# Performance work log

Measured on AMD Instinct MI355X. Metric: run time of the kernel, lower is better.

The kernel has to match this reference:

```python
import jax, jax.numpy as jnp
import numpy as np

NUM_HEADS = 8
NEG_SLOPE = 0.2


def setup_inputs() -> dict:
    key = jax.random.key(0)
    k1, k2, k3, k4 = jax.random.split(key, 4)
    B, N, D_IN, D_K, D_V = 4, 4096, 256, 256, 256
    x = jax.random.normal(k1, (B, N, D_IN), dtype=jnp.float32)
    Wq = jax.random.normal(k2, (D_IN, D_K), dtype=jnp.float32) * (1.0 / np.sqrt(D_IN))
    Wk = jax.random.normal(k3, (D_IN, D_K), dtype=jnp.float32) * (1.0 / np.sqrt(D_IN))
    Wv = jax.random.normal(k4, (D_IN, D_V), dtype=jnp.float32) * (1.0 / np.sqrt(D_IN))
    return {"x": x, "Wq": Wq, "Wk": Wk, "Wv": Wv}


def reference(x, Wq, Wk, Wv):
    B, N, _ = x.shape
    nh = NUM_HEADS
    dim_k = Wq.shape[1]
    dim_v = Wv.shape[1]
    dk, dv = dim_k // nh, dim_v // nh
    nor_fact = 1.0 / np.sqrt(dk)
    # project and split heads: [B, H, N, dk]
    q = (x @ Wq).reshape(B, N, nh, dk).transpose(0, 2, 1, 3)
    k = (x @ Wk).reshape(B, N, nh, dk).transpose(0, 2, 1, 3)
    v = (x @ Wv).reshape(B, N, nh, dv).transpose(0, 2, 1, 3)
    # all-pairs scores, scaled then LeakyReLU (no softmax)
    dist = jnp.einsum('bhnd,bhmd->bhnm', q, k) * nor_fact
    dist = jnp.where(dist >= 0, dist, NEG_SLOPE * dist)
    att = jnp.einsum('bhnm,bhmd->bhnd', dist, v)
    return att.transpose(0, 2, 1, 3).reshape(B, N, dim_v)
```

## Files before the change

### kernel.cpp

```cpp
#include <hip/hip_runtime.h>

typedef __attribute__((ext_vector_type(8))) short short8;
typedef __attribute__((ext_vector_type(4))) float f32x4;
typedef __attribute__((ext_vector_type(2))) unsigned int u32x2;
typedef __attribute__((ext_vector_type(4))) unsigned int u32x4;

#define MFMA16x32(A, B, C) \
  __builtin_amdgcn_mfma_f32_16x16x32_bf16((A), (B), (C), 0, 0, 0)

__device__ __forceinline__ void async_cp16(const unsigned short* g, void* l) {
  __builtin_amdgcn_global_load_lds(
      (const __attribute__((address_space(1))) unsigned int*)g,
      (__attribute__((address_space(3))) unsigned int*)l, 16, 0, 0);
}

__device__ __forceinline__ unsigned int fbits(float f) {
  return __builtin_bit_cast(unsigned int, f);
}
__device__ __forceinline__ unsigned int pack_bf16(float a, float b) {
  return __builtin_amdgcn_perm(fbits(b), fbits(a), 0x07060302u);
}
__device__ __forceinline__ unsigned short bf16_rne(float f) {
  unsigned int u = fbits(f);
  return (unsigned short)((u + 0x8000u) >> 16);
}

__global__ __launch_bounds__(256) void prep_kernel(
    const float* __restrict__ x, unsigned short* __restrict__ xb,
    const float* __restrict__ Wq, const float* __restrict__ Wk,
    const float* __restrict__ Wv, unsigned short* __restrict__ WT) {
  __shared__ float tile[32][33];
  if (blockIdx.x < 4096) {
    const size_t i = ((size_t)blockIdx.x * 256 + threadIdx.x) * 4;
    const float4 f = *(const float4*)(x + i);
    u32x2 u = {(unsigned int)bf16_rne(f.x) | ((unsigned int)bf16_rne(f.y) << 16),
               (unsigned int)bf16_rne(f.z) | ((unsigned int)bf16_rne(f.w) << 16)};
    *(u32x2*)(xb + i) = u;
    return;
  }
  const int bid = blockIdx.x - 4096;
  const int g = bid / 64, rem = bid % 64;
  const int k0 = (rem >> 3) * 32, n0 = (rem & 7) * 32;
  const float* W = (g == 0) ? Wq : (g == 1) ? Wk : Wv;
  const int t = threadIdx.x;
  {
    const int kr = t >> 3, nc = (t & 7) * 4;
    const float4 f = *(const float4*)(W + (size_t)(k0 + kr) * 256 + n0 + nc);
    tile[kr][nc + 0] = f.x; tile[kr][nc + 1] = f.y;
    tile[kr][nc + 2] = f.z; tile[kr][nc + 3] = f.w;
  }
  __syncthreads();
  {
    const int nr = t >> 3, kc = (t & 7) * 4;
    unsigned int u0 = (unsigned int)bf16_rne(tile[kc + 0][nr]) |
                      ((unsigned int)bf16_rne(tile[kc + 1][nr]) << 16);
    unsigned int u1 = (unsigned int)bf16_rne(tile[kc + 2][nr]) |
                      ((unsigned int)bf16_rne(tile[kc + 3][nr]) << 16);
    u32x2 u = {u0, u1};
    *(u32x2*)(WT + (size_t)g * 65536 + (size_t)(n0 + nr) * 256 + k0 + kc) = u;
  }
}

__global__ __launch_bounds__(256, 2) void proj_kernel(
    const unsigned short* __restrict__ xb, const unsigned short* __restrict__ WT,
    unsigned short* __restrict__ QH, unsigned short* __restrict__ KH,
    unsigned short* __restrict__ VT) {
  __shared__ __align__(16) char smem[65536];
  const int tid = threadIdx.x;
  const int w = tid >> 6, lane = tid & 63, l15 = lane & 15, quad = lane >> 4;
  const int bid = blockIdx.x;
  const int mtile = bid / 6, nt = bid % 6;
  const int g = nt >> 1, n0 = (nt & 1) * 128;
  const int m0 = mtile * 128;

  const int srow = lane >> 3, useg = lane & 7;
  const int swz = (useg ^ srow) * 8;
  const unsigned short* aS = xb + (size_t)(m0 + w * 32 + srow) * 256 + swz;
  const unsigned short* bS =
      WT + (size_t)g * 65536 + (size_t)(n0 + w * 32 + srow) * 256 + swz;

#pragma unroll
  for (int j = 0; j < 4; j++) {
    async_cp16(aS + j * 2048, smem + w * 4096 + j * 1024);
    async_cp16(bS + j * 2048, smem + 16384 + w * 4096 + j * 1024);
  }
  __syncthreads();

  const f32x4 zero = {0.f, 0.f, 0.f, 0.f};
  f32x4 acc[2][8];
#pragma unroll
  for (int s = 0; s < 2; s++)
#pragma unroll
    for (int c = 0; c < 8; c++) acc[s][c] = zero;

  const int sw = l15 & 7;
  for (int t = 0; t < 4; t++) {
    const int nb = t & 1;
    const int kn = ((t + 1) & 3) * 64;
#pragma unroll
    for (int j = 0; j < 4; j++) {
      async_cp16(aS + kn + j * 2048,
                 smem + (nb ^ 1) * 32768 + w * 4096 + j * 1024);
      async_cp16(bS + kn + j * 2048,
                 smem + (nb ^ 1) * 32768 + 16384 + w * 4096 + j * 1024);
    }
    const char* Ab = smem + nb * 32768;
    const char* Bb = Ab + 16384;
#pragma unroll
    for (int ks = 0; ks < 2; ks++) {
      const int seg = ((ks * 4 + quad) ^ sw) * 16;
      short8 af[2], bf[8];
#pragma unroll
      for (int s = 0; s < 2; s++)
        af[s] = *(const short8*)(Ab + (w * 32 + s * 16 + l15) * 128 + seg);
#pragma unroll
      for (int c = 0; c < 8; c++)
        bf[c] = *(const short8*)(Bb + (c * 16 + l15) * 128 + seg);
      if (g < 2) {
#pragma unroll
        for (int s = 0; s < 2; s++)
#pragma unroll
          for (int c = 0; c < 8; c++)
            acc[s][c] = MFMA16x32(bf[c], af[s], acc[s][c]);
      } else {
#pragma unroll
        for (int s = 0; s < 2; s++)
#pragma unroll
          for (int c = 0; c < 8; c++)
            acc[s][c] = MFMA16x32(af[s], bf[c], acc[s][c]);
      }
    }
    __syncthreads();
  }

  if (g < 2) {
    unsigned short* O = g ? KH : QH;
    const float sc = g ? 1.0f : 0.17677669529663688f;
#pragma unroll
    for (int s = 0; s < 2; s++)
#pragma unroll
      for (int c = 0; c < 8; c++) {
        const int row = m0 + w * 32 + s * 16 + l15;
        const int col = n0 + c * 16 + quad * 4;
        const int bb = row >> 12, nn = row & 4095;
        const int hh = col >> 5, dl = col & 31;
        u32x2 pk = {pack_bf16(acc[s][c][0] * sc, acc[s][c][1] * sc),
                    pack_bf16(acc[s][c][2] * sc, acc[s][c][3] * sc)};
        *(u32x2*)(O + ((size_t)(bb * 8 + hh) * 4096 + nn) * 32 + dl) = pk;
      }
  } else {
#pragma unroll
    for (int s = 0; s < 2; s++)
#pragma unroll
      for (int c = 0; c < 8; c++) {
        const int col = n0 + c * 16 + l15;
        const int hh = col >> 5, dl = col & 31;
        const int row = m0 + w * 32 + s * 16 + quad * 4;
        const int bb = row >> 12;
        const int nn = (row & 4064) | (quad << 3) | ((s & 1) << 2);
        u32x2 pk = {pack_bf16(acc[s][c][0], acc[s][c][1]),
                    pack_bf16(acc[s][c][2], acc[s][c][3])};
        *(u32x2*)(VT + (size_t)((bb * 8 + hh) * 32 + dl) * 4096 + nn) = pk;
      }
  }
}

__global__ __launch_bounds__(512, 4) void attn_kernel(
    const unsigned short* __restrict__ QH, const unsigned short* __restrict__ KH,
    const unsigned short* __restrict__ VT, float* __restrict__ out) {
  __shared__ __align__(16) char smem[16384];
  const int tid = threadIdx.x;
  const int w = tid >> 6, lane = tid & 63, l15 = lane & 15, quad = lane >> 4;
  const int bid = blockIdx.x;
  const int bh = bid & 31, qh = bid >> 5;
  const int b = bh >> 3, h = bh & 7;
  const int qbase = qh * 256 + w * 32;

  const unsigned short* Qp =
      QH + ((size_t)bh * 4096 + qbase + l15) * 32 + quad * 8;
  short8 qf[2];
#pragma unroll
  for (int s = 0; s < 2; s++) qf[s] = *(const short8*)(Qp + (size_t)s * 512);

  const bool isK = (w < 4);
  const unsigned short* src0;
  int kstr, wbOff;
  if (isK) {
    const int key = w * 16 + (lane >> 2);
    const int gseg = (lane & 3) ^ ((lane >> 3) & 3);
    src0 = KH + ((size_t)bh * 4096 + key) * 32 + gseg * 8;
    kstr = 32;
    wbOff = w * 1024;
  } else {
    const int r = (w - 4) * 8 + (lane >> 3), useg = lane & 7;
    src0 = VT + ((size_t)bh * 32 + r) * 4096 + ((useg ^ (r & 7)) * 8);
    kstr = 1;
    wbOff = 4096 + (w - 4) * 1024;
  }

  async_cp16(src0, smem + wbOff);
  __syncthreads();

  const f32x4 zero = {0.f, 0.f, 0.f, 0.f};
  f32x4 acc[2][2];
#pragma unroll
  for (int s = 0; s < 2; s++) {
    acc[s][0] = zero;
    acc[s][1] = zero;
  }

  const int rs = l15 & 7;
  const int kseg = (quad ^ ((l15 >> 1) & 3)) * 16;
  for (int i = 0; i < 64; i++) {
    const int nb = i & 1;
    const int kn = ((i + 1) & 63) * 64;
    async_cp16(src0 + (size_t)kn * kstr, smem + (nb ^ 1) * 8192 + wbOff);

    const char* Kb = smem + nb * 8192;
    const char* Vb = Kb + 4096;
    short8 kf[4];
#pragma unroll
    for (int c = 0; c < 4; c++)
      kf[c] = *(const short8*)(Kb + (c * 16 + l15) * 64 + kseg);
    short8 vf[2][2];
#pragma unroll
    for (int dt = 0; dt < 2; dt++) {
      const char* Vr = Vb + (dt * 16 + l15) * 128;
#pragma unroll
      for (int u = 0; u < 2; u++)
        vf[dt][u] = *(const short8*)(Vr + (((4 * u + quad) ^ rs) * 16));
    }

#pragma unroll
    for (int s = 0; s < 2; s++) {
      unsigned int pp[4][2];
#pragma unroll
      for (int c = 0; c < 4; c++) {
        f32x4 st = MFMA16x32(kf[c], qf[s], zero);
        float t0 = fmaxf(st[0], 0.2f * st[0]);
        float t1 = fmaxf(st[1], 0.2f * st[1]);
        float t2 = fmaxf(st[2], 0.2f * st[2]);
        float t3 = fmaxf(st[3], 0.2f * st[3]);
        pp[c][0] = pack_bf16(t0, t1);
        pp[c][1] = pack_bf16(t2, t3);
      }
#pragma unroll
      for (int u = 0; u < 2; u++) {
        u32x4 bw = {pp[2 * u][0], pp[2 * u][1],
                    pp[2 * u + 1][0], pp[2 * u + 1][1]};
        short8 pb = __builtin_bit_cast(short8, bw);
#pragma unroll
        for (int dt = 0; dt < 2; dt++)
          acc[s][dt] = MFMA16x32(vf[dt][u], pb, acc[s][dt]);
      }
    }
    __syncthreads();
  }

#pragma unroll
  for (int s = 0; s < 2; s++)
#pragma unroll
    for (int dt = 0; dt < 2; dt++)
      *(f32x4*)(out + ((size_t)b * 4096 + qbase + s * 16 + l15) * 256 + h * 32 +
                dt * 16 + quad * 4) = acc[s][dt];
}

extern "C" void kernel_launch(void* const* d_in, const int* in_sizes, int n_in,
                              void* d_out, int out_size, void* d_ws,
                              size_t ws_size, hipStream_t stream) {
  const float* x = (const float*)d_in[0];
  const float* Wq = (const float*)d_in[1];
  const float* Wk = (const float*)d_in[2];
  const float* Wv = (const float*)d_in[3];
  float* out = (float*)d_out;

  unsigned short* ws = (unsigned short*)d_ws;
  unsigned short* QHb = ws;
  unsigned short* KHb = ws + 4194304;
  unsigned short* VTb = ws + 2 * 4194304;
  unsigned short* xbb = ws + 3 * 4194304;
  unsigned short* WTb = ws + 4 * 4194304;

  prep_kernel<<<4288, 256, 0, stream>>>(x, xbb, Wq, Wk, Wv, WTb);
  proj_kernel<<<768, 256, 0, stream>>>(xbb, WTb, QHb, KHb, VTb);
  attn_kernel<<<512, 512, 0, stream>>>(QHb, KHb, VTb, out);
}
```

Before: 168.6 us.

## Halve per-wave query rows in attention, double grid, raise occupancy bound

Each wave of the attention kernel now covers 16 query rows instead of 32. The grid doubles to 1024 blocks and the launch bound targets 8 blocks per CU. LeakyReLU is also rewritten as a packed 2-wide multiply and max before the bf16 pack. The aim is more parallelism and better latency hiding, but every block now streams all K/V tiles for half as many queries. That doubles K/V global and LDS traffic per unit of work and halves MFMA reuse of each loaded K/V fragment.

```diff
diff --git a/kernel.cpp b/kernel.cpp
--- a/kernel.cpp
+++ b/kernel.cpp
@@ -2,6 +2,7 @@
 
 typedef __attribute__((ext_vector_type(8))) short short8;
 typedef __attribute__((ext_vector_type(4))) float f32x4;
+typedef __attribute__((ext_vector_type(2))) float f32x2;
 typedef __attribute__((ext_vector_type(2))) unsigned int u32x2;
 typedef __attribute__((ext_vector_type(4))) unsigned int u32x4;
 
@@ -23,6 +24,12 @@
 __device__ __forceinline__ unsigned short bf16_rne(float f) {
   unsigned int u = fbits(f);
   return (unsigned short)((u + 0x8000u) >> 16);
+}
+__device__ __forceinline__ unsigned int leaky_pack(float a, float b) {
+  f32x2 v = {a, b};
+  f32x2 m = v * 0.2f;
+  f32x2 r = __builtin_elementwise_max(v, m);
+  return pack_bf16(r[0], r[1]);
 }
 
 __global__ __launch_bounds__(256) void prep_kernel(
@@ -165,7 +172,7 @@
   }
 }
 
-__global__ __launch_bounds__(512, 4) void attn_kernel(
+__global__ __launch_bounds__(512, 8) void attn_kernel(
     const unsigned short* __restrict__ QH, const unsigned short* __restrict__ KH,
     const unsigned short* __restrict__ VT, float* __restrict__ out) {
   __shared__ __align__(16) char smem[16384];
@@ -174,13 +181,11 @@
   const int bid = blockIdx.x;
   const int bh = bid & 31, qh = bid >> 5;
   const int b = bh >> 3, h = bh & 7;
-  const int qbase = qh * 256 + w * 32;
+  const int qbase = qh * 128 + w * 16;
 
   const unsigned short* Qp =
       QH + ((size_t)bh * 4096 + qbase + l15) * 32 + quad * 8;
-  short8 qf[2];
-#pragma unroll
-  for (int s = 0; s < 2; s++) qf[s] = *(const short8*)(Qp + (size_t)s * 512);
+  const short8 qf = *(const short8*)Qp;
 
   const bool isK = (w < 4);
   const unsigned short* src0;
@@ -202,12 +207,9 @@
   __syncthreads();
 
   const f32x4 zero = {0.f, 0.f, 0.f, 0.f};
-  f32x4 acc[2][2];
-#pragma unroll
-  for (int s = 0; s < 2; s++) {
-    acc[s][0] = zero;
-    acc[s][1] = zero;
-  }
+  f32x4 acc[2];
+  acc[0] = zero;
+  acc[1] = zero;
 
   const int rs = l15 & 7;
   const int kseg = (quad ^ ((l15 >> 1) & 3)) * 16;
@@ -231,38 +233,29 @@
         vf[dt][u] = *(const short8*)(Vr + (((4 * u + quad) ^ rs) * 16));
     }
 
-#pragma unroll
-    for (int s = 0; s < 2; s++) {
-      unsigned int pp[4][2];
-#pragma unroll
-      for (int c = 0; c < 4; c++) {
-        f32x4 st = MFMA16x32(kf[c], qf[s], zero);
-        float t0 = fmaxf(st[0], 0.2f * st[0]);
-        float t1 = fmaxf(st[1], 0.2f * st[1]);
-        float t2 = fmaxf(st[2], 0.2f * st[2]);
-        float t3 = fmaxf(st[3], 0.2f * st[3]);
-        pp[c][0] = pack_bf16(t0, t1);
-        pp[c][1] = pack_bf16(t2, t3);
-      }
-#pragma unroll
-      for (int u = 0; u < 2; u++) {
-        u32x4 bw = {pp[2 * u][0], pp[2 * u][1],
-                    pp[2 * u + 1][0], pp[2 * u + 1][1]};
-        short8 pb = __builtin_bit_cast(short8, bw);
-#pragma unroll
-        for (int dt = 0; dt < 2; dt++)
-          acc[s][dt] = MFMA16x32(vf[dt][u], pb, acc[s][dt]);
-      }
+    unsigned int pp[4][2];
+#pragma unroll
+    for (int c = 0; c < 4; c++) {
+      f32x4 st = MFMA16x32(kf[c], qf, zero);
+      pp[c][0] = leaky_pack(st[0], st[1]);
+      pp[c][1] = leaky_pack(st[2], st[3]);
+    }
+#pragma unroll
+    for (int u = 0; u < 2; u++) {
+      u32x4 bw = {pp[2 * u][0], pp[2 * u][1],
+                  pp[2 * u + 1][0], pp[2 * u + 1][1]};
+      short8 pb = __builtin_bit_cast(short8, bw);
+#pragma unroll
+      for (int dt = 0; dt < 2; dt++)
+        acc[dt] = MFMA16x32(vf[dt][u], pb, acc[dt]);
     }
     __syncthreads();
   }
 
 #pragma unroll
-  for (int s = 0; s < 2; s++)
-#pragma unroll
-    for (int dt = 0; dt < 2; dt++)
-      *(f32x4*)(out + ((size_t)b * 4096 + qbase + s * 16 + l15) * 256 + h * 32 +
-                dt * 16 + quad * 4) = acc[s][dt];
+  for (int dt = 0; dt < 2; dt++)
+    *(f32x4*)(out + ((size_t)b * 4096 + qbase + l15) * 256 + h * 32 +
+              dt * 16 + quad * 4) = acc[dt];
 }
 
 extern "C" void kernel_launch(void* const* d_in, const int* in_sizes, int n_in,
@@ -283,5 +276,5 @@
 
   prep_kernel<<<4288, 256, 0, stream>>>(x, xbb, Wq, Wk, Wv, WTb);
   proj_kernel<<<768, 256, 0, stream>>>(xbb, WTb, QHb, KHb, VTb);
-  attn_kernel<<<512, 512, 0, stream>>>(QHb, KHb, VTb, out);
-}
+  attn_kernel<<<1024, 512, 0, stream>>>(QHb, KHb, VTb, out);
+}
```

Result: slower. 185.6 us (+10.1%).

## Decompose LeakyReLU into ReLU plus linear term via precomputed V^T K

Applied to the files above, without the earlier changes.

Rewrites LeakyReLU(s) as 0.8*ReLU(s) + 0.2*s. The linear part is computed once per block as q·(K^T V) from a 32x32 matrix M that every block builds from the full K and V, and the inner loop then needs only a packed-bf16 integer max against zero. This cuts the per-score VALU work (multiply, max, separate pack) down to pack plus one packed max. The cost is that each block re-reads all of K and V for its head to build M, using strided scalar K loads, a larger shared buffer, and extra syncs.

```diff
diff --git a/kernel.cpp b/kernel.cpp
--- a/kernel.cpp
+++ b/kernel.cpp
@@ -23,6 +23,11 @@
 __device__ __forceinline__ unsigned short bf16_rne(float f) {
   unsigned int u = fbits(f);
   return (unsigned short)((u + 0x8000u) >> 16);
+}
+__device__ __forceinline__ unsigned int relu_pk_bf16(unsigned int x) {
+  unsigned int r;
+  asm("v_pk_max_i16 %0, %1, 0" : "=v"(r) : "v"(x));
+  return r;
 }
 
 __global__ __launch_bounds__(256) void prep_kernel(
@@ -168,7 +173,7 @@
 __global__ __launch_bounds__(512, 4) void attn_kernel(
     const unsigned short* __restrict__ QH, const unsigned short* __restrict__ KH,
     const unsigned short* __restrict__ VT, float* __restrict__ out) {
-  __shared__ __align__(16) char smem[16384];
+  __shared__ __align__(16) char smem[32768];
   const int tid = threadIdx.x;
   const int w = tid >> 6, lane = tid & 63, l15 = lane & 15, quad = lane >> 4;
   const int bid = blockIdx.x;
@@ -181,6 +186,67 @@
   short8 qf[2];
 #pragma unroll
   for (int s = 0; s < 2; s++) qf[s] = *(const short8*)(Qp + (size_t)s * 512);
+
+  const f32x4 zero = {0.f, 0.f, 0.f, 0.f};
+
+  float* Mred = (float*)smem;
+  {
+    f32x4 mm[2][2];
+#pragma unroll
+    for (int dt = 0; dt < 2; dt++)
+#pragma unroll
+      for (int it = 0; it < 2; it++) mm[dt][it] = zero;
+    const unsigned short* Vg = VT + ((size_t)bh * 32 + l15) * 4096 + quad * 8;
+    const unsigned short* Kg = KH + ((size_t)bh * 4096) * 32 + l15;
+    for (int g = 0; g < 16; g++) {
+      const int kb = w * 512 + g * 32;
+      short8 va[2];
+#pragma unroll
+      for (int dt = 0; dt < 2; dt++)
+        va[dt] = *(const short8*)(Vg + (size_t)dt * 16 * 4096 + kb);
+      short8 kv[2];
+#pragma unroll
+      for (int it = 0; it < 2; it++) {
+        unsigned short t[8];
+#pragma unroll
+        for (int j = 0; j < 8; j++)
+          t[j] = Kg[(size_t)(kb + (j >> 2) * 16 + quad * 4 + (j & 3)) * 32 +
+                    it * 16];
+        kv[it] = *(const short8*)t;
+      }
+#pragma unroll
+      for (int dt = 0; dt < 2; dt++)
+#pragma unroll
+        for (int it = 0; it < 2; it++)
+          mm[dt][it] = MFMA16x32(va[dt], kv[it], mm[dt][it]);
+    }
+#pragma unroll
+    for (int dt = 0; dt < 2; dt++)
+#pragma unroll
+      for (int it = 0; it < 2; it++)
+#pragma unroll
+        for (int r = 0; r < 4; r++)
+          Mred[w * 1024 + (dt * 16 + quad * 4 + r) * 32 + it * 16 + l15] =
+              mm[dt][it][r];
+  }
+  __syncthreads();
+  short8 ma[2];
+  {
+#pragma unroll
+    for (int dt = 0; dt < 2; dt++) {
+      f32x4 sa = zero, sb = zero;
+#pragma unroll
+      for (int ww = 0; ww < 8; ww++) {
+        const float* p = Mred + ww * 1024 + (dt * 16 + l15) * 32 + quad * 8;
+        sa += *(const f32x4*)p;
+        sb += *(const f32x4*)(p + 4);
+      }
+      u32x4 mw = {pack_bf16(sa[0], sa[1]), pack_bf16(sa[2], sa[3]),
+                  pack_bf16(sb[0], sb[1]), pack_bf16(sb[2], sb[3])};
+      ma[dt] = __builtin_bit_cast(short8, mw);
+    }
+  }
+  __syncthreads();
 
   const bool isK = (w < 4);
   const unsigned short* src0;
@@ -201,7 +267,6 @@
   async_cp16(src0, smem + wbOff);
   __syncthreads();
 
-  const f32x4 zero = {0.f, 0.f, 0.f, 0.f};
   f32x4 acc[2][2];
 #pragma unroll
   for (int s = 0; s < 2; s++) {
@@ -237,12 +302,8 @@
 #pragma unroll
       for (int c = 0; c < 4; c++) {
         f32x4 st = MFMA16x32(kf[c], qf[s], zero);
-        float t0 = fmaxf(st[0], 0.2f * st[0]);
-        float t1 = fmaxf(st[1], 0.2f * st[1]);
-        float t2 = fmaxf(st[2], 0.2f * st[2]);
-        float t3 = fmaxf(st[3], 0.2f * st[3]);
-        pp[c][0] = pack_bf16(t0, t1);
-        pp[c][1] = pack_bf16(t2, t3);
+        pp[c][0] = relu_pk_bf16(pack_bf16(st[0], st[1]));
+        pp[c][1] = relu_pk_bf16(pack_bf16(st[2], st[3]));
       }
 #pragma unroll
       for (int u = 0; u < 2; u++) {
@@ -260,9 +321,12 @@
 #pragma unroll
   for (int s = 0; s < 2; s++)
 #pragma unroll
-    for (int dt = 0; dt < 2; dt++)
+    for (int dt = 0; dt < 2; dt++) {
+      f32x4 corr = MFMA16x32(ma[dt], qf[s], zero);
+      f32x4 o = acc[s][dt] * 0.8f + corr * 0.2f;
       *(f32x4*)(out + ((size_t)b * 4096 + qbase + s * 16 + l15) * 256 + h * 32 +
-                dt * 16 + quad * 4) = acc[s][dt];
+                dt * 16 + quad * 4) = o;
+    }
 }
 
 extern "C" void kernel_launch(void* const* d_in, const int* in_sizes, int n_in,
```

New measurement: 180.6 us. 1.07x slower.
